# Kernel optimization log

Measured on AMD Instinct MI355X. Metric: run time of the kernel, lower is better.

The kernel has to match this reference:

```python
import jax, jax.numpy as jnp
import numpy as np

DIM = 1024
NUM_HEADS = 8
HEAD_DIM = 64
INNER = NUM_HEADS * HEAD_DIM  # 512


def setup_inputs() -> dict:
    key = jax.random.key(0)
    ks = jax.random.split(key, 7)
    B, N, M = 8, 512, 4096
    x = jax.random.normal(ks[0], (B, N, DIM), dtype=jnp.float32)
    context = jax.random.normal(ks[1], (B, M, DIM), dtype=jnp.float32)
    s_in = 1.0 / np.sqrt(DIM)
    s_inner = 1.0 / np.sqrt(INNER)
    # Linear weights stored as [in, out] for x @ W
    Wq = jax.random.normal(ks[2], (DIM, INNER), dtype=jnp.float32) * s_in
    Wk = jax.random.normal(ks[3], (DIM, INNER), dtype=jnp.float32) * s_in
    Wv = jax.random.normal(ks[4], (DIM, INNER), dtype=jnp.float32) * s_in
    Wo = jax.random.normal(ks[5], (INNER, DIM), dtype=jnp.float32) * s_inner
    bo = jax.random.normal(ks[6], (DIM,), dtype=jnp.float32) * 0.01
    return {"x": x, "context": context, "Wq": Wq, "Wk": Wk, "Wv": Wv, "Wo": Wo, "bo": bo}


def reference(x, context, Wq, Wk, Wv, Wo, bo):
    B, N, _ = x.shape
    M = context.shape[1]
    scale = HEAD_DIM ** -0.5
    # project and split heads: [B, H, N, D]
    q = (x @ Wq).reshape(B, N, NUM_HEADS, HEAD_DIM).transpose(0, 2, 1, 3)
    k = (context @ Wk).reshape(B, M, NUM_HEADS, HEAD_DIM).transpose(0, 2, 1, 3)
    v = (context @ Wv).reshape(B, M, NUM_HEADS, HEAD_DIM).transpose(0, 2, 1, 3)
    # full attention matrix [B, H, N, M] as in the original module
    attn = jax.nn.softmax(jnp.einsum('bhnd,bhmd->bhnm', q, k) * scale, axis=-1)
    out = jnp.einsum('bhnm,bhmd->bhnd', attn, v)  # [B, H, N, D]
    out = out.transpose(0, 2, 1, 3).reshape(B, N, INNER)
    return out @ Wo + bo
```

## Files before the change

### kernel.cpp

```cpp
#include <hip/hip_runtime.h>
#include <hip/hip_bf16.h>

#define B_SZ 8
#define N_Q 512
#define M_KV 4096
#define DIM 1024
#define INNER 512
#define NHEADS 8
#define HDIM 64

typedef __attribute__((ext_vector_type(4))) float floatx4;
typedef __attribute__((ext_vector_type(8))) short shortx8;
typedef __attribute__((ext_vector_type(4))) short shortx4;

__device__ inline unsigned short f2bf(float f) {
  union { float f; unsigned u; } x; x.f = f;
  unsigned r = x.u + 0x7FFFu + ((x.u >> 16) & 1u);
  return (unsigned short)(r >> 16);
}

__device__ inline shortx8 cvt8(floatx4 a, floatx4 b) {
  shortx8 h;
  h[0] = (short)f2bf(a[0]); h[1] = (short)f2bf(a[1]);
  h[2] = (short)f2bf(a[2]); h[3] = (short)f2bf(a[3]);
  h[4] = (short)f2bf(b[0]); h[5] = (short)f2bf(b[1]);
  h[6] = (short)f2bf(b[2]); h[7] = (short)f2bf(b[3]);
  return h;
}

__device__ inline void gload16(const void* g, void* l) {
  __builtin_amdgcn_global_load_lds(
      (const __attribute__((address_space(1))) void*)g,
      (__attribute__((address_space(3))) void*)l, 16, 0, 0);
}

__global__ void k_cvt_bf16(const float* __restrict__ src,
                           unsigned short* __restrict__ dst, long n) {
  long stride = (long)gridDim.x * 256 * 8;
  for (long i = ((long)blockIdx.x * 256 + threadIdx.x) * 8; i < n; i += stride) {
    floatx4 a = *reinterpret_cast<const floatx4*>(src + i);
    floatx4 b = *reinterpret_cast<const floatx4*>(src + i + 4);
    *reinterpret_cast<shortx8*>(dst + i) = cvt8(a, b);
  }
}

__global__ void k_transpose_bf16(const float* __restrict__ W,
                                 unsigned short* __restrict__ Wt,
                                 int K, int N) {
  __shared__ unsigned short t[32][36];
  const int kt = blockIdx.x * 32, nt = blockIdx.y * 32;
  const int tr = threadIdx.x >> 3;
  const int tc = (threadIdx.x & 7) * 4;
  floatx4 v = *reinterpret_cast<const floatx4*>(&W[(long)(kt + tr) * N + nt + tc]);
  #pragma unroll
  for (int j = 0; j < 4; ++j) t[tr][tc + j] = f2bf(v[j]);
  __syncthreads();
  shortx4 o;
  #pragma unroll
  for (int j = 0; j < 4; ++j) o[j] = (short)t[tc + j][tr];
  *reinterpret_cast<shortx4*>(&Wt[(long)(nt + tr) * K + kt + tc]) = o;
}

__global__ __launch_bounds__(256, 4)
void k_gemm_kv(const unsigned short* __restrict__ Ah,
               const unsigned short* __restrict__ Wkvt,
               unsigned short* __restrict__ Kh,
               unsigned short* __restrict__ Vt) {
  __shared__ unsigned short As[2][128 * 32];
  __shared__ unsigned short Bs[2][128 * 32];
  const int tid = threadIdx.x;
  const int lane = tid & 63;
  const int w = tid >> 6;
  const int wr = w >> 1, wc = w & 1;
  const int fr = lane & 15, fc = lane >> 4;

  const int L = ((blockIdx.x & 7) << 8) + (blockIdx.x >> 3);
  const int mt = L >> 3, nt = L & 7;
  const long arow0 = (long)mt << 7;
  const long bcol0 = (long)nt << 7;

  const int grow = lane >> 2;
  const int gpos = lane & 3;

  floatx4 acc[4][4] = {};

  #define STAGE(buf, kt)                                                      \
    {                                                                         \
      _Pragma("unroll")                                                       \
      for (int g = 0; g < 2; ++g) {                                           \
        const int rl = w * 32 + g * 16 + grow;                                \
        const int cc = gpos ^ ((rl >> 1) & 3);                                \
        gload16(Ah + (arow0 + rl) * 1024 + (kt) + cc * 8,                     \
                &As[buf][(w * 32 + g * 16) * 32]);                            \
        gload16(Wkvt + (bcol0 + rl) * 1024 + (kt) + cc * 8,                   \
                &Bs[buf][(w * 32 + g * 16) * 32]);                            \
      }                                                                       \
    }

  STAGE(0, 0);
  __syncthreads();

  for (int i = 0; i < 32; ++i) {
    const int cur = i & 1;
    if (i < 31) STAGE(cur ^ 1, (i + 1) << 5);

    shortx8 af[4], bf[4];
    #pragma unroll
    for (int rb = 0; rb < 4; ++rb) {
      int row = wr * 64 + rb * 16 + fr;
      af[rb] = *reinterpret_cast<const shortx8*>(
          &As[cur][row * 32 + ((fc ^ ((row >> 1) & 3)) * 8)]);
    }
    #pragma unroll
    for (int cb = 0; cb < 4; ++cb) {
      int row = wc * 64 + cb * 16 + fr;
      bf[cb] = *reinterpret_cast<const shortx8*>(
          &Bs[cur][row * 32 + ((fc ^ ((row >> 1) & 3)) * 8)]);
    }
    __builtin_amdgcn_s_setprio(1);
    #pragma unroll
    for (int rb = 0; rb < 4; ++rb) {
      #pragma unroll
      for (int cb = 0; cb < 4; ++cb)
        acc[rb][cb] = __builtin_amdgcn_mfma_f32_16x16x32_bf16(
            af[rb], bf[cb], acc[rb][cb], 0, 0, 0);
    }
    __builtin_amdgcn_s_setprio(0);
    __syncthreads();
  }
  #undef STAGE

  #pragma unroll
  for (int rb = 0; rb < 4; ++rb) {
    #pragma unroll
    for (int cb = 0; cb < 4; ++cb) {
      long gr0 = arow0 + wr * 64 + rb * 16 + fc * 4;
      long gc = bcol0 + wc * 64 + cb * 16 + fr;
      long b = gr0 >> 12, m = gr0 & 4095;
      if (gc < 512) {
        long h = gc >> 6, d = gc & 63;
        #pragma unroll
        for (int r = 0; r < 4; ++r)
          Kh[((((b * 8 + h) << 12) + m + r) << 6) + d] = f2bf(acc[rb][cb][r]);
      } else {
        long h = (gc - 512) >> 6, d = (gc - 512) & 63;
        shortx4 hv;
        #pragma unroll
        for (int r = 0; r < 4; ++r) hv[r] = (short)f2bf(acc[rb][cb][r]);
        *reinterpret_cast<shortx4*>(&Vt[(((b * 8 + h) * 64 + d) << 12) + m]) = hv;
      }
    }
  }
}

template<int MODE, bool ABF, int NCOL, int MBITS>
__global__ __launch_bounds__(512, 4)
void k_gemm(const void* __restrict__ Ap, const unsigned short* __restrict__ Bt,
            void* __restrict__ Cout, const float* __restrict__ bias,
            int M, int N, int K, float oscale) {
  __shared__ unsigned short As[2][128 * 32];
  __shared__ unsigned short Bs[2][256 * 32];
  const int tid = threadIdx.x;
  const int lane = tid & 63;
  const int w = tid >> 6;
  const int wr = w >> 2, wc = w & 3;

  const int cpx = gridDim.x >> 3;
  const int L = (blockIdx.x & 7) * cpx + (blockIdx.x >> 3);
  const long arow0 = (long)(L / NCOL) * 128;
  const long bcol0 = (long)(L % NCOL) * 256;

  const float* Af = (const float*)Ap;
  const unsigned short* Ah = (const unsigned short*)Ap;

  const int lsub = lane >> 2;
  const int lchunk = (lane & 3) ^ ((lane >> 3) & 3);
  const long brow0 = bcol0 + (w * 2 + 0) * 16 + lsub;
  const long brow1 = bcol0 + (w * 2 + 1) * 16 + lsub;
  const long ahrow = arow0 + w * 16 + lsub;
  const int arow = tid >> 2;
  const int acseg = tid & 3;
  const int aswz = arow * 32 + ((acseg ^ ((arow >> 1) & 3)) * 8);

  floatx4 acc[4][4] = {};

  #define STAGE_B(buf, kt)                                                   \
    {                                                                        \
      gload16(Bt + brow0 * K + (kt) + lchunk * 8, &Bs[buf][(w * 2) * 512]);  \
      gload16(Bt + brow1 * K + (kt) + lchunk * 8,                            \
              &Bs[buf][(w * 2 + 1) * 512]);                                  \
    }
  #define STAGE_AH(buf, kt) \
    gload16(Ah + ahrow * K + (kt) + lchunk * 8, &As[buf][w * 512]);

  if (ABF) {
    STAGE_AH(0, 0);
  } else {
    const float* src = Af + (arow0 + arow) * (long)K + acseg * 8;
    floatx4 a0 = *reinterpret_cast<const floatx4*>(src);
    floatx4 a1 = *reinterpret_cast<const floatx4*>(src + 4);
    *reinterpret_cast<shortx8*>(&As[0][aswz]) = cvt8(a0, a1);
  }
  STAGE_B(0, 0);
  __syncthreads();

  const int NK = K >> 5;
  for (int i = 0; i < NK; ++i) {
    const int cur = i & 1;
    const bool more = (i + 1) < NK;
    floatx4 a0, a1;
    if (more) {
      const long ktn = (long)(i + 1) << 5;
      if (ABF) {
        STAGE_AH(cur ^ 1, ktn);
      } else {
        const float* src = Af + (arow0 + arow) * (long)K + ktn + acseg * 8;
        a0 = *reinterpret_cast<const floatx4*>(src);
        a1 = *reinterpret_cast<const floatx4*>(src + 4);
      }
      STAGE_B(cur ^ 1, ktn);
    }

    shortx8 af[4], bf[4];
    #pragma unroll
    for (int rb = 0; rb < 4; ++rb) {
      int row = wr * 64 + rb * 16 + (lane & 15);
      af[rb] = *reinterpret_cast<const shortx8*>(
          &As[cur][row * 32 + (((lane >> 4) ^ ((row >> 1) & 3)) * 8)]);
    }
    #pragma unroll
    for (int cb = 0; cb < 4; ++cb) {
      int row = wc * 64 + cb * 16 + (lane & 15);
      bf[cb] = *reinterpret_cast<const shortx8*>(
          &Bs[cur][row * 32 + (((lane >> 4) ^ ((row >> 1) & 3)) * 8)]);
    }
    #pragma unroll
    for (int rb = 0; rb < 4; ++rb) {
      #pragma unroll
      for (int cb = 0; cb < 4; ++cb)
        acc[rb][cb] = __builtin_amdgcn_mfma_f32_16x16x32_bf16(
            af[rb], bf[cb], acc[rb][cb], 0, 0, 0);
    }

    if (more && !ABF)
      *reinterpret_cast<shortx8*>(&As[cur ^ 1][aswz]) = cvt8(a0, a1);
    __syncthreads();
  }
  #undef STAGE_B
  #undef STAGE_AH

  #pragma unroll
  for (int rb = 0; rb < 4; ++rb) {
    #pragma unroll
    for (int cb = 0; cb < 4; ++cb) {
      long gr0 = arow0 + wr * 64 + rb * 16 + (lane >> 4) * 4;
      long gc  = bcol0 + wc * 64 + cb * 16 + (lane & 15);
      if (MODE == 0) {
        float bv = bias[gc];
        #pragma unroll
        for (int r = 0; r < 4; ++r)
          ((float*)Cout)[(gr0 + r) * N + gc] = acc[rb][cb][r] + bv;
      } else if (MODE == 2) {
        long b = gr0 >> MBITS, m = gr0 & ((1 << MBITS) - 1);
        long h = gc >> 6, d = gc & 63;
        #pragma unroll
        for (int r = 0; r < 4; ++r)
          ((unsigned short*)Cout)[((((b * 8 + h) << MBITS) + m + r) << 6) + d] =
              f2bf(acc[rb][cb][r] * oscale);
      }
    }
  }
}

__global__ __launch_bounds__(256, 2)
void k_attn(const unsigned short* __restrict__ Qh,
            const unsigned short* __restrict__ Kh,
            const unsigned short* __restrict__ Vt,
            unsigned short* __restrict__ Aout) {
  __shared__ unsigned short Ks[64][72];
  __shared__ unsigned short Vs[64][72];
  __shared__ unsigned short QPs[64][72];
  const int tid = threadIdx.x;
  const int lane = tid & 63;
  const int w = tid >> 6;
  const int wg = blockIdx.x;
  const int bh = wg & 63;
  const int qt = wg >> 6;
  const int b = bh >> 3, h = bh & 7;

  const unsigned short* Qbase = Qh + (((long)bh << 9) + qt * 64) * 64;
  const unsigned short* Kbase = Kh + (((long)bh) << 18);
  const unsigned short* Vbase = Vt + (((long)bh) << 18);

  const int sr = tid >> 2;
  const int sc = (tid & 3) * 16;

  {
    const unsigned short* src = Qbase + sr * 64 + sc;
    *reinterpret_cast<shortx8*>(&QPs[sr][sc]) =
        *reinterpret_cast<const shortx8*>(src);
    *reinterpret_cast<shortx8*>(&QPs[sr][sc + 8]) =
        *reinterpret_cast<const shortx8*>(src + 8);
  }
  {
    const unsigned short* ksrc = Kbase + sr * 64 + sc;
    *reinterpret_cast<shortx8*>(&Ks[sr][sc]) =
        *reinterpret_cast<const shortx8*>(ksrc);
    *reinterpret_cast<shortx8*>(&Ks[sr][sc + 8]) =
        *reinterpret_cast<const shortx8*>(ksrc + 8);
    const unsigned short* vsrc = Vbase + ((long)sr << 12) + sc;
    *reinterpret_cast<shortx8*>(&Vs[sr][sc]) =
        *reinterpret_cast<const shortx8*>(vsrc);
    *reinterpret_cast<shortx8*>(&Vs[sr][sc + 8]) =
        *reinterpret_cast<const shortx8*>(vsrc + 8);
  }
  __syncthreads();

  shortx8 qf[2];
  qf[0] = *reinterpret_cast<const shortx8*>(
      &QPs[w * 16 + (lane & 15)][(lane >> 4) * 8]);
  qf[1] = *reinterpret_cast<const shortx8*>(
      &QPs[w * 16 + (lane & 15)][32 + (lane >> 4) * 8]);

  floatx4 o_acc[4] = {};
  float l_part[4] = {0.f, 0.f, 0.f, 0.f};
  shortx8 kpre[2], vpre[2];

  for (int mt = 0; mt < M_KV / 64; ++mt) {
    if (mt < M_KV / 64 - 1) {
      const unsigned short* ksrc = Kbase + ((mt + 1) * 64 + sr) * 64 + sc;
      kpre[0] = *reinterpret_cast<const shortx8*>(ksrc);
      kpre[1] = *reinterpret_cast<const shortx8*>(ksrc + 8);
      const unsigned short* vsrc = Vbase + ((long)sr << 12) + (mt + 1) * 64 + sc;
      vpre[0] = *reinterpret_cast<const shortx8*>(vsrc);
      vpre[1] = *reinterpret_cast<const shortx8*>(vsrc + 8);
    }

    floatx4 s[4];
    #pragma unroll
    for (int cb = 0; cb < 4; ++cb) {
      shortx8 k0 = *reinterpret_cast<const shortx8*>(
          &Ks[cb * 16 + (lane & 15)][(lane >> 4) * 8]);
      shortx8 k1 = *reinterpret_cast<const shortx8*>(
          &Ks[cb * 16 + (lane & 15)][32 + (lane >> 4) * 8]);
      floatx4 z = {};
      z = __builtin_amdgcn_mfma_f32_16x16x32_bf16(qf[0], k0, z, 0, 0, 0);
      s[cb] = __builtin_amdgcn_mfma_f32_16x16x32_bf16(qf[1], k1, z, 0, 0, 0);
    }

    #pragma unroll
    for (int cb = 0; cb < 4; ++cb) {
      #pragma unroll
      for (int r = 0; r < 4; ++r) {
        float pv = __expf(s[cb][r]);
        l_part[r] += pv;
        QPs[w * 16 + (lane >> 4) * 4 + r][cb * 16 + (lane & 15)] = f2bf(pv);
      }
    }

    #pragma unroll
    for (int kk = 0; kk < 2; ++kk) {
      shortx8 pf = *reinterpret_cast<const shortx8*>(
          &QPs[w * 16 + (lane & 15)][kk * 32 + (lane >> 4) * 8]);
      #pragma unroll
      for (int db = 0; db < 4; ++db) {
        shortx8 vf = *reinterpret_cast<const shortx8*>(
            &Vs[db * 16 + (lane & 15)][kk * 32 + (lane >> 4) * 8]);
        o_acc[db] = __builtin_amdgcn_mfma_f32_16x16x32_bf16(
            pf, vf, o_acc[db], 0, 0, 0);
      }
    }

    __syncthreads();
    if (mt < M_KV / 64 - 1) {
      *reinterpret_cast<shortx8*>(&Ks[sr][sc]) = kpre[0];
      *reinterpret_cast<shortx8*>(&Ks[sr][sc + 8]) = kpre[1];
      *reinterpret_cast<shortx8*>(&Vs[sr][sc]) = vpre[0];
      *reinterpret_cast<shortx8*>(&Vs[sr][sc + 8]) = vpre[1];
      __syncthreads();
    }
  }

  float inv[4];
  #pragma unroll
  for (int r = 0; r < 4; ++r) {
    float l = l_part[r];
    l += __shfl_xor(l, 1);
    l += __shfl_xor(l, 2);
    l += __shfl_xor(l, 4);
    l += __shfl_xor(l, 8);
    inv[r] = 1.f / l;
  }
  #pragma unroll
  for (int db = 0; db < 4; ++db) {
    #pragma unroll
    for (int r = 0; r < 4; ++r) {
      int n = qt * 64 + w * 16 + (lane >> 4) * 4 + r;
      long idx = ((long)(b * N_Q + n)) * INNER + h * HDIM + db * 16 + (lane & 15);
      Aout[idx] = f2bf(o_acc[db][r] * inv[r]);
    }
  }
}

extern "C" void kernel_launch(void* const* d_in, const int* in_sizes, int n_in,
                              void* d_out, int out_size, void* d_ws, size_t ws_size,
                              hipStream_t stream) {
  const float* x   = (const float*)d_in[0];
  const float* ctx = (const float*)d_in[1];
  const float* Wq  = (const float*)d_in[2];
  const float* Wk  = (const float*)d_in[3];
  const float* Wv  = (const float*)d_in[4];
  const float* Wo  = (const float*)d_in[5];
  const float* bo  = (const float*)d_in[6];
  float* out = (float*)d_out;

  char* ws = (char*)d_ws;
  unsigned short* Qh   = (unsigned short*)(ws);
  unsigned short* Kh   = (unsigned short*)(ws + (4ull  << 20));
  unsigned short* Vt   = (unsigned short*)(ws + (36ull << 20));
  unsigned short* ctxh = (unsigned short*)(ws + (68ull << 20));
  unsigned short* Aat  = (unsigned short*)(ws + (68ull << 20));
  unsigned short* Wqt  = (unsigned short*)(ws + (132ull << 20));
  unsigned short* Wkvt = (unsigned short*)(ws + (133ull << 20));
  unsigned short* Wot  = (unsigned short*)(ws + (135ull << 20));

  k_cvt_bf16<<<dim3(2048), dim3(256), 0, stream>>>(
      ctx, ctxh, (long)B_SZ * M_KV * DIM);

  k_transpose_bf16<<<dim3(DIM / 32, INNER / 32), dim3(256), 0, stream>>>(
      Wq, Wqt, DIM, INNER);
  k_transpose_bf16<<<dim3(DIM / 32, INNER / 32), dim3(256), 0, stream>>>(
      Wk, Wkvt, DIM, INNER);
  k_transpose_bf16<<<dim3(DIM / 32, INNER / 32), dim3(256), 0, stream>>>(
      Wv, Wkvt + (size_t)INNER * DIM, DIM, INNER);
  k_transpose_bf16<<<dim3(INNER / 32, DIM / 32), dim3(256), 0, stream>>>(
      Wo, Wot, INNER, DIM);

  k_gemm<2, false, 2, 9><<<dim3(64), dim3(512), 0, stream>>>(
      x, Wqt, Qh, nullptr, B_SZ * N_Q, INNER, DIM, 0.125f);

  k_gemm_kv<<<dim3(2048), dim3(256), 0, stream>>>(ctxh, Wkvt, Kh, Vt);

  k_attn<<<dim3(B_SZ * NHEADS * (N_Q / 64)), dim3(256), 0, stream>>>(Qh, Kh, Vt, Aat);

  k_gemm<0, true, 4, 0><<<dim3(128), dim3(512), 0, stream>>>(
      Aat, Wot, out, bo, B_SZ * N_Q, DIM, INNER, 1.0f);
}
```

Before: 256.0 us.

## Enlarge KV GEMM tiles, deepen pipeline, merge weight transposes, prioritize attention MFMAs

The K/V projection GEMM moves from 128x128 tiles with 256 threads and double buffering to 256x256 tiles with 512 threads and a four-stage global_load_lds pipeline. It uses explicit vmcnt waits and raw barriers in place of __syncthreads. The four weight-transpose launches become one 3D-grid launch, and the attention kernel raises wave priority around its MFMA sections. The goal is more data reuse per loaded tile, more latency hiding and less launch overhead. The cost is higher register and LDS use (8x4 accumulators and 128KB of LDS) with lower occupancy.

```diff
diff --git a/kernel.cpp b/kernel.cpp
--- a/kernel.cpp
+++ b/kernel.cpp
@@ -44,10 +44,23 @@
   }
 }
 
-__global__ void k_transpose_bf16(const float* __restrict__ W,
-                                 unsigned short* __restrict__ Wt,
-                                 int K, int N) {
+__global__ void k_transpose_all(const float* __restrict__ Wq,
+                                const float* __restrict__ Wk,
+                                const float* __restrict__ Wv,
+                                const float* __restrict__ Wo,
+                                unsigned short* __restrict__ Wqt,
+                                unsigned short* __restrict__ Wkvt,
+                                unsigned short* __restrict__ Wot) {
   __shared__ unsigned short t[32][36];
+  const int z = blockIdx.z;
+  const float* W;
+  unsigned short* Wt;
+  int K, N;
+  if (z == 0)      { W = Wq; Wt = Wqt;  K = 1024; N = 512; }
+  else if (z == 1) { W = Wk; Wt = Wkvt; K = 1024; N = 512; }
+  else if (z == 2) { W = Wv; Wt = Wkvt + (size_t)512 * 1024; K = 1024; N = 512; }
+  else             { W = Wo; Wt = Wot;  K = 512;  N = 1024; }
+  if ((int)blockIdx.x * 32 >= K || (int)blockIdx.y * 32 >= N) return;
   const int kt = blockIdx.x * 32, nt = blockIdx.y * 32;
   const int tr = threadIdx.x >> 3;
   const int tc = (threadIdx.x & 7) * 4;
@@ -61,93 +74,102 @@
   *reinterpret_cast<shortx4*>(&Wt[(long)(nt + tr) * K + kt + tc]) = o;
 }
 
-__global__ __launch_bounds__(256, 4)
+__global__ __launch_bounds__(512, 2)
 void k_gemm_kv(const unsigned short* __restrict__ Ah,
                const unsigned short* __restrict__ Wkvt,
                unsigned short* __restrict__ Kh,
                unsigned short* __restrict__ Vt) {
-  __shared__ unsigned short As[2][128 * 32];
-  __shared__ unsigned short Bs[2][128 * 32];
+  __shared__ unsigned short As[4][8192];
+  __shared__ unsigned short Bs[4][8192];
   const int tid = threadIdx.x;
   const int lane = tid & 63;
   const int w = tid >> 6;
-  const int wr = w >> 1, wc = w & 1;
+  const int wr = w >> 2, wc = w & 3;
   const int fr = lane & 15, fc = lane >> 4;
 
-  const int L = ((blockIdx.x & 7) << 8) + (blockIdx.x >> 3);
-  const int mt = L >> 3, nt = L & 7;
-  const long arow0 = (long)mt << 7;
-  const long bcol0 = (long)nt << 7;
+  const int L = ((blockIdx.x & 7) << 6) + (blockIdx.x >> 3);
+  const int mt = L >> 2, nt = L & 3;
+  const long arow0 = (long)mt << 8;
+  const long bcol0 = (long)nt << 8;
 
   const int grow = lane >> 2;
-  const int gpos = lane & 3;
-
-  floatx4 acc[4][4] = {};
-
-  #define STAGE(buf, kt)                                                      \
-    {                                                                         \
-      _Pragma("unroll")                                                       \
-      for (int g = 0; g < 2; ++g) {                                           \
-        const int rl = w * 32 + g * 16 + grow;                                \
-        const int cc = gpos ^ ((rl >> 1) & 3);                                \
-        gload16(Ah + (arow0 + rl) * 1024 + (kt) + cc * 8,                     \
-                &As[buf][(w * 32 + g * 16) * 32]);                            \
-        gload16(Wkvt + (bcol0 + rl) * 1024 + (kt) + cc * 8,                   \
-                &Bs[buf][(w * 32 + g * 16) * 32]);                            \
-      }                                                                       \
-    }
+  const int gchunk = (lane & 3) ^ ((lane >> 3) & 3);
+
+  floatx4 acc[8][4] = {};
+
+  #define STAGE(buf, kt_)                                                \
+    { _Pragma("unroll")                                                  \
+      for (int j = 0; j < 2; ++j) {                                      \
+        const int rl = j * 128 + w * 16 + grow;                          \
+        gload16(Ah + (arow0 + rl) * 1024 + (kt_) + gchunk * 8,           \
+                &As[buf][(j * 128 + w * 16) * 32]);                      \
+        gload16(Wkvt + (bcol0 + rl) * 1024 + (kt_) + gchunk * 8,         \
+                &Bs[buf][(j * 128 + w * 16) * 32]);                      \
+      } }
 
   STAGE(0, 0);
-  __syncthreads();
-
-  for (int i = 0; i < 32; ++i) {
-    const int cur = i & 1;
-    if (i < 31) STAGE(cur ^ 1, (i + 1) << 5);
-
-    shortx8 af[4], bf[4];
-    #pragma unroll
-    for (int rb = 0; rb < 4; ++rb) {
-      int row = wr * 64 + rb * 16 + fr;
-      af[rb] = *reinterpret_cast<const shortx8*>(
+  STAGE(1, 32);
+  STAGE(2, 64);
+
+  for (int t = 0; t < 32; ++t) {
+    const int cur = t & 3;
+    if (t < 29) {
+      STAGE((t + 3) & 3, (t + 3) << 5);
+      asm volatile("s_waitcnt vmcnt(12)" ::: "memory");
+    } else if (t == 29) {
+      asm volatile("s_waitcnt vmcnt(8)" ::: "memory");
+    } else if (t == 30) {
+      asm volatile("s_waitcnt vmcnt(4)" ::: "memory");
+    } else {
+      asm volatile("s_waitcnt vmcnt(0)" ::: "memory");
+    }
+    __builtin_amdgcn_s_barrier();
+
+    shortx8 bf[4], af[8];
+    #pragma unroll
+    for (int n = 0; n < 4; ++n) {
+      int row = wc * 64 + n * 16 + fr;
+      bf[n] = *reinterpret_cast<const shortx8*>(
+          &Bs[cur][row * 32 + ((fc ^ ((row >> 1) & 3)) * 8)]);
+    }
+    #pragma unroll
+    for (int m = 0; m < 8; ++m) {
+      int row = wr * 128 + m * 16 + fr;
+      af[m] = *reinterpret_cast<const shortx8*>(
           &As[cur][row * 32 + ((fc ^ ((row >> 1) & 3)) * 8)]);
     }
-    #pragma unroll
-    for (int cb = 0; cb < 4; ++cb) {
-      int row = wc * 64 + cb * 16 + fr;
-      bf[cb] = *reinterpret_cast<const shortx8*>(
-          &Bs[cur][row * 32 + ((fc ^ ((row >> 1) & 3)) * 8)]);
-    }
     __builtin_amdgcn_s_setprio(1);
     #pragma unroll
-    for (int rb = 0; rb < 4; ++rb) {
+    for (int m = 0; m < 8; ++m) {
       #pragma unroll
-      for (int cb = 0; cb < 4; ++cb)
-        acc[rb][cb] = __builtin_amdgcn_mfma_f32_16x16x32_bf16(
-            af[rb], bf[cb], acc[rb][cb], 0, 0, 0);
+      for (int n = 0; n < 4; ++n)
+        acc[m][n] = __builtin_amdgcn_mfma_f32_16x16x32_bf16(
+            af[m], bf[n], acc[m][n], 0, 0, 0);
     }
     __builtin_amdgcn_s_setprio(0);
-    __syncthreads();
+    asm volatile("s_waitcnt lgkmcnt(0)" ::: "memory");
+    __builtin_amdgcn_s_barrier();
   }
   #undef STAGE
 
   #pragma unroll
-  for (int rb = 0; rb < 4; ++rb) {
-    #pragma unroll
-    for (int cb = 0; cb < 4; ++cb) {
-      long gr0 = arow0 + wr * 64 + rb * 16 + fc * 4;
-      long gc = bcol0 + wc * 64 + cb * 16 + fr;
-      long b = gr0 >> 12, m = gr0 & 4095;
+  for (int m = 0; m < 8; ++m) {
+    #pragma unroll
+    for (int n = 0; n < 4; ++n) {
+      long gr0 = arow0 + wr * 128 + m * 16 + fc * 4;
+      long gc = bcol0 + wc * 64 + n * 16 + fr;
+      long b = gr0 >> 12, mm = gr0 & 4095;
       if (gc < 512) {
         long h = gc >> 6, d = gc & 63;
         #pragma unroll
         for (int r = 0; r < 4; ++r)
-          Kh[((((b * 8 + h) << 12) + m + r) << 6) + d] = f2bf(acc[rb][cb][r]);
+          Kh[((((b * 8 + h) << 12) + mm + r) << 6) + d] = f2bf(acc[m][n][r]);
       } else {
         long h = (gc - 512) >> 6, d = (gc - 512) & 63;
         shortx4 hv;
         #pragma unroll
-        for (int r = 0; r < 4; ++r) hv[r] = (short)f2bf(acc[rb][cb][r]);
-        *reinterpret_cast<shortx4*>(&Vt[(((b * 8 + h) * 64 + d) << 12) + m]) = hv;
+        for (int r = 0; r < 4; ++r) hv[r] = (short)f2bf(acc[m][n][r]);
+        *reinterpret_cast<shortx4*>(&Vt[(((b * 8 + h) * 64 + d) << 12) + mm]) = hv;
       }
     }
   }
@@ -337,6 +359,7 @@
     }
 
     floatx4 s[4];
+    __builtin_amdgcn_s_setprio(1);
     #pragma unroll
     for (int cb = 0; cb < 4; ++cb) {
       shortx8 k0 = *reinterpret_cast<const shortx8*>(
@@ -347,6 +370,7 @@
       z = __builtin_amdgcn_mfma_f32_16x16x32_bf16(qf[0], k0, z, 0, 0, 0);
       s[cb] = __builtin_amdgcn_mfma_f32_16x16x32_bf16(qf[1], k1, z, 0, 0, 0);
     }
+    __builtin_amdgcn_s_setprio(0);
 
     #pragma unroll
     for (int cb = 0; cb < 4; ++cb) {
@@ -358,6 +382,7 @@
       }
     }
 
+    __builtin_amdgcn_s_setprio(1);
     #pragma unroll
     for (int kk = 0; kk < 2; ++kk) {
       shortx8 pf = *reinterpret_cast<const shortx8*>(
@@ -370,6 +395,7 @@
             pf, vf, o_acc[db], 0, 0, 0);
       }
     }
+    __builtin_amdgcn_s_setprio(0);
 
     __syncthreads();
     if (mt < M_KV / 64 - 1) {
@@ -427,19 +453,13 @@
   k_cvt_bf16<<<dim3(2048), dim3(256), 0, stream>>>(
       ctx, ctxh, (long)B_SZ * M_KV * DIM);
 
-  k_transpose_bf16<<<dim3(DIM / 32, INNER / 32), dim3(256), 0, stream>>>(
-      Wq, Wqt, DIM, INNER);
-  k_transpose_bf16<<<dim3(DIM / 32, INNER / 32), dim3(256), 0, stream>>>(
-      Wk, Wkvt, DIM, INNER);
-  k_transpose_bf16<<<dim3(DIM / 32, INNER / 32), dim3(256), 0, stream>>>(
-      Wv, Wkvt + (size_t)INNER * DIM, DIM, INNER);
-  k_transpose_bf16<<<dim3(INNER / 32, DIM / 32), dim3(256), 0, stream>>>(
-      Wo, Wot, INNER, DIM);
+  k_transpose_all<<<dim3(32, 32, 4), dim3(256), 0, stream>>>(
+      Wq, Wk, Wv, Wo, Wqt, Wkvt, Wot);
 
   k_gemm<2, false, 2, 9><<<dim3(64), dim3(512), 0, stream>>>(
       x, Wqt, Qh, nullptr, B_SZ * N_Q, INNER, DIM, 0.125f);
 
-  k_gemm_kv<<<dim3(2048), dim3(256), 0, stream>>>(ctxh, Wkvt, Kh, Vt);
+  k_gemm_kv<<<dim3(512), dim3(512), 0, stream>>>(ctxh, Wkvt, Kh, Vt);
 
   k_attn<<<dim3(B_SZ * NHEADS * (N_Q / 64)), dim3(256), 0, stream>>>(Qh, Kh, Vt, Aat);
 
```

Measured after the change: 260.5 us. About the same (+1.8%).

## Split attention over KV halves with async LDS double-buffering and a reduce kernel

Applied to the files above, without the earlier changes.

Splits the attention KV loop into two halves across twice as many workgroups and writes unnormalised fp32 partial outputs and row sums. A new reduce kernel combines the halves, normalises and writes bf16. K/V tiles are double-buffered in LDS through direct global-to-LDS loads with an XOR swizzle, MFMA sections are bracketed by setprio, and the four weight transposes are merged into one launch. This aims to fill more CUs and hide load latency, at the cost of an extra launch and about 16MB of fp32 partial traffic.

```diff
diff --git a/kernel.cpp b/kernel.cpp
--- a/kernel.cpp
+++ b/kernel.cpp
@@ -44,10 +44,23 @@
   }
 }
 
-__global__ void k_transpose_bf16(const float* __restrict__ W,
-                                 unsigned short* __restrict__ Wt,
-                                 int K, int N) {
+__global__ void k_transpose_all(const float* __restrict__ Wq,
+                                const float* __restrict__ Wk,
+                                const float* __restrict__ Wv,
+                                const float* __restrict__ Wo,
+                                unsigned short* __restrict__ Wqt,
+                                unsigned short* __restrict__ Wkvt,
+                                unsigned short* __restrict__ Wot) {
   __shared__ unsigned short t[32][36];
+  const int z = blockIdx.z;
+  const float* W;
+  unsigned short* Wt;
+  int K, N;
+  if (z == 0)      { W = Wq; Wt = Wqt;  K = 1024; N = 512; }
+  else if (z == 1) { W = Wk; Wt = Wkvt; K = 1024; N = 512; }
+  else if (z == 2) { W = Wv; Wt = Wkvt + (size_t)512 * 1024; K = 1024; N = 512; }
+  else             { W = Wo; Wt = Wot;  K = 512;  N = 1024; }
+  if ((int)blockIdx.x * 32 >= K || (int)blockIdx.y * 32 >= N) return;
   const int kt = blockIdx.x * 32, nt = blockIdx.y * 32;
   const int tr = threadIdx.x >> 3;
   const int tc = (threadIdx.x & 7) * 4;
@@ -272,81 +285,81 @@
   }
 }
 
-__global__ __launch_bounds__(256, 2)
+__global__ __launch_bounds__(256, 3)
 void k_attn(const unsigned short* __restrict__ Qh,
             const unsigned short* __restrict__ Kh,
             const unsigned short* __restrict__ Vt,
-            unsigned short* __restrict__ Aout) {
-  __shared__ unsigned short Ks[64][72];
-  __shared__ unsigned short Vs[64][72];
-  __shared__ unsigned short QPs[64][72];
+            float* __restrict__ Opart, float* __restrict__ Lpart) {
+  __shared__ unsigned short Qs[64 * 64];
+  __shared__ unsigned short Ks[2][64 * 64];
+  __shared__ unsigned short Vs[2][64 * 64];
+  __shared__ unsigned short Ps[64][72];
   const int tid = threadIdx.x;
   const int lane = tid & 63;
   const int w = tid >> 6;
   const int wg = blockIdx.x;
   const int bh = wg & 63;
-  const int qt = wg >> 6;
-  const int b = bh >> 3, h = bh & 7;
+  const int qt = (wg >> 6) & 7;
+  const int sp = wg >> 9;
+  const int fr = lane & 15, fc = lane >> 4;
 
   const unsigned short* Qbase = Qh + (((long)bh << 9) + qt * 64) * 64;
   const unsigned short* Kbase = Kh + (((long)bh) << 18);
   const unsigned short* Vbase = Vt + (((long)bh) << 18);
 
-  const int sr = tid >> 2;
-  const int sc = (tid & 3) * 16;
-
+  const int grow = lane >> 3;
+  const int gpos = lane & 7;
+
+  #define STAGE_KV(buf, mt_)                                              \
+    { _Pragma("unroll")                                                   \
+      for (int j = 0; j < 2; ++j) {                                       \
+        const int r = w * 16 + j * 8 + grow;                              \
+        const int c = gpos ^ (r & 7);                                     \
+        gload16(Kbase + ((mt_) * 64 + r) * 64 + c * 8,                    \
+                &Ks[buf][(w * 16 + j * 8) * 64]);                         \
+        gload16(Vbase + (((long)r) << 12) + (mt_) * 64 + c * 8,           \
+                &Vs[buf][(w * 16 + j * 8) * 64]);                         \
+      } }
+
+  const int mt0 = sp * 32;
   {
-    const unsigned short* src = Qbase + sr * 64 + sc;
-    *reinterpret_cast<shortx8*>(&QPs[sr][sc]) =
-        *reinterpret_cast<const shortx8*>(src);
-    *reinterpret_cast<shortx8*>(&QPs[sr][sc + 8]) =
-        *reinterpret_cast<const shortx8*>(src + 8);
-  }
-  {
-    const unsigned short* ksrc = Kbase + sr * 64 + sc;
-    *reinterpret_cast<shortx8*>(&Ks[sr][sc]) =
-        *reinterpret_cast<const shortx8*>(ksrc);
-    *reinterpret_cast<shortx8*>(&Ks[sr][sc + 8]) =
-        *reinterpret_cast<const shortx8*>(ksrc + 8);
-    const unsigned short* vsrc = Vbase + ((long)sr << 12) + sc;
-    *reinterpret_cast<shortx8*>(&Vs[sr][sc]) =
-        *reinterpret_cast<const shortx8*>(vsrc);
-    *reinterpret_cast<shortx8*>(&Vs[sr][sc + 8]) =
-        *reinterpret_cast<const shortx8*>(vsrc + 8);
+    #pragma unroll
+    for (int j = 0; j < 2; ++j) {
+      const int r = w * 16 + j * 8 + grow;
+      const int c = gpos ^ (r & 7);
+      gload16(Qbase + r * 64 + c * 8, &Qs[(w * 16 + j * 8) * 64]);
+    }
+    STAGE_KV(0, mt0);
   }
   __syncthreads();
 
   shortx8 qf[2];
-  qf[0] = *reinterpret_cast<const shortx8*>(
-      &QPs[w * 16 + (lane & 15)][(lane >> 4) * 8]);
-  qf[1] = *reinterpret_cast<const shortx8*>(
-      &QPs[w * 16 + (lane & 15)][32 + (lane >> 4) * 8]);
+  #pragma unroll
+  for (int kk = 0; kk < 2; ++kk)
+    qf[kk] = *reinterpret_cast<const shortx8*>(
+        &Qs[(w * 16 + fr) * 64 + (((kk * 4 + fc) ^ (fr & 7)) * 8)]);
 
   floatx4 o_acc[4] = {};
   float l_part[4] = {0.f, 0.f, 0.f, 0.f};
-  shortx8 kpre[2], vpre[2];
-
-  for (int mt = 0; mt < M_KV / 64; ++mt) {
-    if (mt < M_KV / 64 - 1) {
-      const unsigned short* ksrc = Kbase + ((mt + 1) * 64 + sr) * 64 + sc;
-      kpre[0] = *reinterpret_cast<const shortx8*>(ksrc);
-      kpre[1] = *reinterpret_cast<const shortx8*>(ksrc + 8);
-      const unsigned short* vsrc = Vbase + ((long)sr << 12) + (mt + 1) * 64 + sc;
-      vpre[0] = *reinterpret_cast<const shortx8*>(vsrc);
-      vpre[1] = *reinterpret_cast<const shortx8*>(vsrc + 8);
-    }
+
+  for (int it = 0; it < 32; ++it) {
+    const int cur = it & 1;
+    if (it < 31) STAGE_KV(cur ^ 1, mt0 + it + 1);
 
     floatx4 s[4];
-    #pragma unroll
-    for (int cb = 0; cb < 4; ++cb) {
+    __builtin_amdgcn_s_setprio(1);
+    #pragma unroll
+    for (int cb = 0; cb < 4; ++cb) {
+      int row = cb * 16 + fr;
       shortx8 k0 = *reinterpret_cast<const shortx8*>(
-          &Ks[cb * 16 + (lane & 15)][(lane >> 4) * 8]);
+          &Ks[cur][row * 64 + ((fc ^ (fr & 7)) * 8)]);
       shortx8 k1 = *reinterpret_cast<const shortx8*>(
-          &Ks[cb * 16 + (lane & 15)][32 + (lane >> 4) * 8]);
+          &Ks[cur][row * 64 + (((4 + fc) ^ (fr & 7)) * 8)]);
       floatx4 z = {};
       z = __builtin_amdgcn_mfma_f32_16x16x32_bf16(qf[0], k0, z, 0, 0, 0);
       s[cb] = __builtin_amdgcn_mfma_f32_16x16x32_bf16(qf[1], k1, z, 0, 0, 0);
     }
+    __builtin_amdgcn_s_setprio(0);
 
     #pragma unroll
     for (int cb = 0; cb < 4; ++cb) {
@@ -354,34 +367,29 @@
       for (int r = 0; r < 4; ++r) {
         float pv = __expf(s[cb][r]);
         l_part[r] += pv;
-        QPs[w * 16 + (lane >> 4) * 4 + r][cb * 16 + (lane & 15)] = f2bf(pv);
+        Ps[w * 16 + fc * 4 + r][cb * 16 + fr] = f2bf(pv);
       }
     }
 
+    __builtin_amdgcn_s_setprio(1);
     #pragma unroll
     for (int kk = 0; kk < 2; ++kk) {
       shortx8 pf = *reinterpret_cast<const shortx8*>(
-          &QPs[w * 16 + (lane & 15)][kk * 32 + (lane >> 4) * 8]);
+          &Ps[w * 16 + fr][kk * 32 + fc * 8]);
       #pragma unroll
       for (int db = 0; db < 4; ++db) {
+        int row = db * 16 + fr;
         shortx8 vf = *reinterpret_cast<const shortx8*>(
-            &Vs[db * 16 + (lane & 15)][kk * 32 + (lane >> 4) * 8]);
+            &Vs[cur][row * 64 + (((kk * 4 + fc) ^ (fr & 7)) * 8)]);
         o_acc[db] = __builtin_amdgcn_mfma_f32_16x16x32_bf16(
             pf, vf, o_acc[db], 0, 0, 0);
       }
     }
-
+    __builtin_amdgcn_s_setprio(0);
     __syncthreads();
-    if (mt < M_KV / 64 - 1) {
-      *reinterpret_cast<shortx8*>(&Ks[sr][sc]) = kpre[0];
-      *reinterpret_cast<shortx8*>(&Ks[sr][sc + 8]) = kpre[1];
-      *reinterpret_cast<shortx8*>(&Vs[sr][sc]) = vpre[0];
-      *reinterpret_cast<shortx8*>(&Vs[sr][sc + 8]) = vpre[1];
-      __syncthreads();
-    }
-  }
-
-  float inv[4];
+  }
+  #undef STAGE_KV
+
   #pragma unroll
   for (int r = 0; r < 4; ++r) {
     float l = l_part[r];
@@ -389,17 +397,37 @@
     l += __shfl_xor(l, 2);
     l += __shfl_xor(l, 4);
     l += __shfl_xor(l, 8);
-    inv[r] = 1.f / l;
-  }
+    l_part[r] = l;
+  }
+  float* Ob = Opart + (long)wg * 4096;
   #pragma unroll
   for (int db = 0; db < 4; ++db) {
     #pragma unroll
-    for (int r = 0; r < 4; ++r) {
-      int n = qt * 64 + w * 16 + (lane >> 4) * 4 + r;
-      long idx = ((long)(b * N_Q + n)) * INNER + h * HDIM + db * 16 + (lane & 15);
-      Aout[idx] = f2bf(o_acc[db][r] * inv[r]);
-    }
-  }
+    for (int r = 0; r < 4; ++r)
+      Ob[(w * 16 + fc * 4 + r) * 64 + db * 16 + fr] = o_acc[db][r];
+  }
+  if (fr == 0) {
+    #pragma unroll
+    for (int r = 0; r < 4; ++r)
+      Lpart[(long)wg * 64 + w * 16 + fc * 4 + r] = l_part[r];
+  }
+}
+
+__global__ void k_attn_reduce(const float* __restrict__ Opart,
+                              const float* __restrict__ Lpart,
+                              unsigned short* __restrict__ Aat) {
+  const int tid = threadIdx.x;
+  const int g = blockIdx.x * 4 + (tid >> 6);
+  const int d = tid & 63;
+  const int bh = g >> 9, n = g & 511;
+  const int b = bh >> 3, h = bh & 7;
+  const int qt = n >> 6, rr = n & 63;
+  const long i0 = ((long)(qt * 64 + bh)) * 4096 + rr * 64 + d;
+  const long i1 = ((long)(512 + qt * 64 + bh)) * 4096 + rr * 64 + d;
+  const float l = Lpart[(long)(qt * 64 + bh) * 64 + rr] +
+                  Lpart[(long)(512 + qt * 64 + bh) * 64 + rr];
+  const float o = Opart[i0] + Opart[i1];
+  Aat[((long)(b * 512 + n)) * 512 + h * 64 + d] = f2bf(o / l);
 }
 
 extern "C" void kernel_launch(void* const* d_in, const int* in_sizes, int n_in,
@@ -420,6 +448,8 @@
   unsigned short* Vt   = (unsigned short*)(ws + (36ull << 20));
   unsigned short* ctxh = (unsigned short*)(ws + (68ull << 20));
   unsigned short* Aat  = (unsigned short*)(ws + (68ull << 20));
+  float*          Opart= (float*)         (ws + (76ull << 20));
+  float*          Lpart= (float*)         (ws + (92ull << 20));
   unsigned short* Wqt  = (unsigned short*)(ws + (132ull << 20));
   unsigned short* Wkvt = (unsigned short*)(ws + (133ull << 20));
   unsigned short* Wot  = (unsigned short*)(ws + (135ull << 20));
@@ -427,21 +457,16 @@
   k_cvt_bf16<<<dim3(2048), dim3(256), 0, stream>>>(
       ctx, ctxh, (long)B_SZ * M_KV * DIM);
 
-  k_transpose_bf16<<<dim3(DIM / 32, INNER / 32), dim3(256), 0, stream>>>(
-      Wq, Wqt, DIM, INNER);
-  k_transpose_bf16<<<dim3(DIM / 32, INNER / 32), dim3(256), 0, stream>>>(
-      Wk, Wkvt, DIM, INNER);
-  k_transpose_bf16<<<dim3(DIM / 32, INNER / 32), dim3(256), 0, stream>>>(
-      Wv, Wkvt + (size_t)INNER * DIM, DIM, INNER);
-  k_transpose_bf16<<<dim3(INNER / 32, DIM / 32), dim3(256), 0, stream>>>(
-      Wo, Wot, INNER, DIM);
+  k_transpose_all<<<dim3(32, 32, 4), dim3(256), 0, stream>>>(
+      Wq, Wk, Wv, Wo, Wqt, Wkvt, Wot);
 
   k_gemm<2, false, 2, 9><<<dim3(64), dim3(512), 0, stream>>>(
       x, Wqt, Qh, nullptr, B_SZ * N_Q, INNER, DIM, 0.125f);
 
   k_gemm_kv<<<dim3(2048), dim3(256), 0, stream>>>(ctxh, Wkvt, Kh, Vt);
 
-  k_attn<<<dim3(B_SZ * NHEADS * (N_Q / 64)), dim3(256), 0, stream>>>(Qh, Kh, Vt, Aat);
+  k_attn<<<dim3(1024), dim3(256), 0, stream>>>(Qh, Kh, Vt, Opart, Lpart);
+  k_attn_reduce<<<dim3(8192), dim3(256), 0, stream>>>(Opart, Lpart, Aat);
 
   k_gemm<0, true, 4, 0><<<dim3(128), dim3(512), 0, stream>>>(
       Aat, Wot, out, bo, B_SZ * N_Q, DIM, INNER, 1.0f);
```

Result: no change. 259.1 us (+1.2%).
